# Performance work log

Measured on AMD Instinct MI355X. Metric: run time of the kernel, lower is better.

The kernel has to match this reference:

```python
import jax, jax.numpy as jnp
import numpy as np

B = 65536
N_SPARSE = 26
N_DENSE = 13
EMB = 5
VOCAB = 100000
N_EXPERTS = 4
D_IN = N_DENSE + N_SPARSE * EMB  # 143
H1, H2 = 128, 64


def setup_inputs() -> dict:
    key = jax.random.key(0)
    ks = jax.random.split(key, 16)
    s = 0.05
    return {
        "sparse_inputs": jax.random.randint(ks[0], (B, N_SPARSE), 0, VOCAB),
        "dense_inputs": jax.random.normal(ks[1], (B, N_DENSE), dtype=jnp.float32),
        "emb_tables": jax.random.normal(ks[2], (N_SPARSE, VOCAB, EMB), dtype=jnp.float32) * s,
        "expert_W1": jax.random.normal(ks[3], (N_EXPERTS, D_IN, H1), dtype=jnp.float32) * s,
        "expert_b1": jnp.zeros((N_EXPERTS, H1), dtype=jnp.float32),
        "expert_W2": jax.random.normal(ks[4], (N_EXPERTS, H1, H2), dtype=jnp.float32) * s,
        "expert_b2": jnp.zeros((N_EXPERTS, H2), dtype=jnp.float32),
        "gate_finish_W": jax.random.normal(ks[5], (D_IN, N_EXPERTS), dtype=jnp.float32) * s,
        "gate_finish_b": jnp.zeros((N_EXPERTS,), dtype=jnp.float32),
        "gate_like_W": jax.random.normal(ks[6], (D_IN, N_EXPERTS), dtype=jnp.float32) * s,
        "gate_like_b": jnp.zeros((N_EXPERTS,), dtype=jnp.float32),
        "finish_W": jax.random.normal(ks[7], (H2, 1), dtype=jnp.float32) * s,
        "finish_b": jnp.zeros((1,), dtype=jnp.float32),
        "like_W": jax.random.normal(ks[8], (H2, 1), dtype=jnp.float32) * s,
        "like_b": jnp.zeros((1,), dtype=jnp.float32),
    }


def reference(sparse_inputs, dense_inputs, emb_tables, expert_W1, expert_b1,
              expert_W2, expert_b2, gate_finish_W, gate_finish_b,
              gate_like_W, gate_like_b, finish_W, finish_b, like_W, like_b):
    # per-feature embedding lookup: [B, N_SPARSE, EMB]
    feat_idx = jnp.arange(N_SPARSE)[None, :]
    sp_emb = emb_tables[feat_idx, sparse_inputs]
    x = jnp.concatenate([dense_inputs, sp_emb.reshape(sparse_inputs.shape[0], -1)], axis=1)  # [B, D_IN]

    # batched expert MLPs (dropout is inactive at inference)
    h = jax.nn.relu(jnp.einsum('bd,edh->beh', x, expert_W1) + expert_b1)  # [B, E, 128]
    expert_out = jax.nn.relu(jnp.einsum('beh,eho->beo', h, expert_W2) + expert_b2)  # [B, E, 64]

    gate_f = jax.nn.softmax(x @ gate_finish_W + gate_finish_b, axis=-1)  # [B, E]
    gate_l = jax.nn.softmax(x @ gate_like_W + gate_like_b, axis=-1)

    task_finish = jnp.einsum('be,beo->bo', gate_f, expert_out)  # [B, 64]
    task_like = jnp.einsum('be,beo->bo', gate_l, expert_out)

    finish = jax.nn.sigmoid(task_finish @ finish_W + finish_b)  # [B, 1]
    like = jax.nn.sigmoid(task_like @ like_W + like_b)  # [B, 1]
    return finish, like
```

## Files before the change

### kernel.cpp

```cpp
#include <hip/hip_runtime.h>
#include <math.h>

#define NB     65536
#define NSP    26
#define NDN    13
#define EMBD   5
#define VOCAB  100000
#define NE     4
#define DIN    143
#define KPAD   160
#define H1     128
#define H2     64

typedef __attribute__((ext_vector_type(8))) short bf16x8;
typedef __attribute__((ext_vector_type(4))) float f32x4;

__device__ __forceinline__ unsigned short f2bf(float f) {
    unsigned int u = __float_as_uint(f);
    u = (u + 0x7fff + ((u >> 16) & 1)) >> 16;
    return (unsigned short)u;
}

__device__ __forceinline__ unsigned cvtpk(float lo, float hi) {
    unsigned r;
    asm("v_cvt_pk_bf16_f32 %0, %1, %2" : "=v"(r) : "v"(lo), "v"(hi));
    return r;
}

#define E1 (4*8*5*512)
#define E2 (4*4*4*512)
#define E3 (5*512)
#define NWE (E1+E2+E3)
#define GBLKS 1024
#define PBLKS ((NWE+255)/256)


__global__ __launch_bounds__(256)
void gather_pack(const int*   __restrict__ sparse,
                 const float* __restrict__ dense,
                 const float* __restrict__ emb,
                 const float* __restrict__ W1,  const float* __restrict__ W2,
                 const float* __restrict__ gfW, const float* __restrict__ glW,
                 unsigned short* __restrict__ w1p, unsigned short* __restrict__ w2p,
                 unsigned short* __restrict__ gwp, unsigned short* __restrict__ xg)
{
    const int blk = blockIdx.x;
    const int tid = threadIdx.x;
    if (blk < GBLKS) {
        __shared__ int idxs[64 * NSP];
        __shared__ __align__(16) unsigned short xs[64][168];
        const int row0 = blk * 64;

        for (int t = tid; t < 64 * NSP; t += 256)
            idxs[t] = sparse[row0 * NSP + t];
        for (int t = tid; t < 64 * NDN; t += 256) {
            int r = t / NDN, c = t - r * NDN;
            xs[r][c] = f2bf(dense[(row0 + r) * NDN + c]);
        }
        for (int t = tid; t < 64 * (KPAD - DIN); t += 256) {
            int r = t / (KPAD - DIN), c = DIN + (t - r * (KPAD - DIN));
            xs[r][c] = 0;
        }
        __syncthreads();
        for (int t = tid; t < 64 * NSP * EMBD; t += 256) {
            int f = t / (64 * EMBD);
            int rem = t - f * (64 * EMBD);
            int r = rem / EMBD, c = rem - r * EMBD;
            int idx = idxs[r * NSP + f];
            float v = emb[((size_t)f * VOCAB + idx) * EMBD + c];
            xs[r][NDN + f * EMBD + c] = f2bf(v);
        }
        __syncthreads();
        for (int v = tid; v < 4 * 5 * 64; v += 256) {
            int lo = v & 63, chunk = v >> 6;
            int s = chunk % 5, tl = chunk / 5;
            int b = lo & 15, g = lo >> 4;
            bf16x8 val = *(const bf16x8*)&xs[tl * 16 + b][32 * s + 8 * g];
            *(bf16x8*)(xg + ((size_t)((blk * 4 + tl) * 5 + s) * 64 + lo) * 8) = val;
        }
        return;
    }

    int i = (blk - GBLKS) * 256 + tid;
    if (i < E1) {
        int j = i & 7, l = (i >> 3) & 63;
        int rest = i >> 9;
        int s = rest % 5; rest /= 5;
        int nt = rest & 7, e = rest >> 3;
        int b = l & 15, g = l >> 4;
        int k = 32 * s + 8 * g + j;
        int n = nt * 16 + b;
        w1p[i] = (k < DIN) ? f2bf(W1[(e * DIN + k) * H1 + n]) : (unsigned short)0;
        return;
    }
    i -= E1;
    if (i < E2) {
        int j = i & 7, l = (i >> 3) & 63;
        int rest = i >> 9;
        int s = rest & 3; rest >>= 2;
        int ot = rest & 3, e = rest >> 2;
        int b = l & 15, g = l >> 4;
        int k = 32 * s + 8 * g + j;
        int o = ot * 16 + b;
        w2p[i] = f2bf(W2[(e * H1 + k) * H2 + o]);
        return;
    }
    i -= E2;
    if (i < E3) {
        int j = i & 7, l = (i >> 3) & 63;
        int s = i >> 9;
        int b = l & 15, g = l >> 4;
        int k = 32 * s + 8 * g + j;
        float v = 0.f;
        if (k < DIN) {
            if (b < 4)      v = gfW[k * NE + b];
            else if (b < 8) v = glW[k * NE + (b - 4)];
        }
        gwp[i] = f2bf(v);
    }
}

__global__ __launch_bounds__(256, 2)
void mmoe7(const unsigned short* __restrict__ xg,
           const unsigned short* __restrict__ w1p, const float* __restrict__ b1,
           const unsigned short* __restrict__ w2p, const float* __restrict__ b2,
           const unsigned short* __restrict__ gwp,
           const float* __restrict__ gfb, const float* __restrict__ glb,
           const float* __restrict__ fW,  const float* __restrict__ fb,
           const float* __restrict__ lW,  const float* __restrict__ lb,
           float* __restrict__ out)
{
    __shared__ __align__(16) char wlds[57344];
    __shared__ __align__(16) char hsb[16384];
    __shared__ float gts[128][8];

    const int tid  = threadIdx.x;
    const int wid  = tid >> 6;
    const int lane = tid & 63;
    const int b    = lane & 15;
    const int g    = lane >> 4;
    const int t0   = blockIdx.x * 8 + wid * 2;
    const int swz  = (b & 7) << 4;
    char* const hw = hsb + wid * 4096 + b * 128;

    bf16x8 xf[2][5];
    #pragma unroll
    for (int rt = 0; rt < 2; ++rt)
        #pragma unroll
        for (int s = 0; s < 5; ++s)
            xf[rt][s] = *(const bf16x8*)(xg + ((size_t)((t0 + rt) * 5 + s) * 64 + lane) * 8);

    bf16x8 pw1[10], pw2[4];
    #pragma unroll
    for (int i = 0; i < 10; ++i)
        pw1[i] = *(const bf16x8*)(w1p + (size_t)(tid + i * 256) * 8);
    #pragma unroll
    for (int i = 0; i < 4; ++i)
        pw2[i] = *(const bf16x8*)(w2p + (size_t)(tid + i * 256) * 8);

    f32x4 ga[2];
    ga[0] = (f32x4){0.f, 0.f, 0.f, 0.f};
    ga[1] = (f32x4){0.f, 0.f, 0.f, 0.f};
    #pragma unroll
    for (int s = 0; s < 5; ++s) {
        bf16x8 af = *(const bf16x8*)(gwp + (size_t)(s * 64 + lane) * 8);
        ga[0] = __builtin_amdgcn_mfma_f32_16x16x32_bf16(af, xf[0][s], ga[0], 0, 0, 0);
        ga[1] = __builtin_amdgcn_mfma_f32_16x16x32_bf16(af, xf[1][s], ga[1], 0, 0, 0);
    }
    if (g < 2) {
        const float4 bias = *(const float4*)(g ? glb : gfb);
        #pragma unroll
        for (int rt = 0; rt < 2; ++rt) {
            float l0 = ga[rt][0] + bias.x, l1 = ga[rt][1] + bias.y;
            float l2 = ga[rt][2] + bias.z, l3 = ga[rt][3] + bias.w;
            float m = fmaxf(fmaxf(l0, l1), fmaxf(l2, l3));
            float e0 = expf(l0 - m), e1 = expf(l1 - m), e2 = expf(l2 - m), e3 = expf(l3 - m);
            float inv = 1.f / (e0 + e1 + e2 + e3);
            float4 gv; gv.x = e0 * inv; gv.y = e1 * inv; gv.z = e2 * inv; gv.w = e3 * inv;
            *(float4*)&gts[wid * 32 + rt * 16 + b][g * 4] = gv;
        }
    }

    float vf[2] = {0.f, 0.f}, vl[2] = {0.f, 0.f};
    for (int e = 0; e < NE; ++e) {
        __syncthreads();
        #pragma unroll
        for (int i = 0; i < 10; ++i)
            *(bf16x8*)(wlds + (tid + i * 256) * 16) = pw1[i];
        #pragma unroll
        for (int i = 0; i < 4; ++i)
            *(bf16x8*)(wlds + 40960 + (tid + i * 256) * 16) = pw2[i];
        if (e < 3) {
            #pragma unroll
            for (int i = 0; i < 10; ++i)
                pw1[i] = *(const bf16x8*)(w1p + (size_t)(e + 1) * 20480 + (size_t)(tid + i * 256) * 8);
            #pragma unroll
            for (int i = 0; i < 4; ++i)
                pw2[i] = *(const bf16x8*)(w2p + (size_t)(e + 1) * 8192 + (size_t)(tid + i * 256) * 8);
        }
        __syncthreads();

        f32x4 c[2][4];
        #pragma unroll
        for (int rt = 0; rt < 2; ++rt)
            #pragma unroll
            for (int ot = 0; ot < 4; ++ot)
                c[rt][ot] = (f32x4){0.f, 0.f, 0.f, 0.f};

        #pragma unroll
        for (int h = 0; h < 2; ++h) {
            #pragma unroll
            for (int nl = 0; nl < 4; ++nl) {
                const int nt = h * 4 + nl;
                bf16x8 wv[5];
                #pragma unroll
                for (int s = 0; s < 5; ++s)
                    wv[s] = *(const bf16x8*)(wlds + ((nt * 5 + s) * 64 + lane) * 16);
                f32x4 acc[2];
                acc[0] = (f32x4){0.f, 0.f, 0.f, 0.f};
                acc[1] = (f32x4){0.f, 0.f, 0.f, 0.f};
                #pragma unroll
                for (int s = 0; s < 5; ++s) {
                    acc[0] = __builtin_amdgcn_mfma_f32_16x16x32_bf16(wv[s], xf[0][s], acc[0], 0, 0, 0);
                    acc[1] = __builtin_amdgcn_mfma_f32_16x16x32_bf16(wv[s], xf[1][s], acc[1], 0, 0, 0);
                }
                const float4 b1v = *(const float4*)(b1 + e * H1 + nt * 16 + 4 * g);
                #pragma unroll
                for (int rt = 0; rt < 2; ++rt) {
                    uint2 hv;
                    hv.x = cvtpk(fmaxf(acc[rt][0] + b1v.x, 0.f), fmaxf(acc[rt][1] + b1v.y, 0.f));
                    hv.y = cvtpk(fmaxf(acc[rt][2] + b1v.z, 0.f), fmaxf(acc[rt][3] + b1v.w, 0.f));
                    *(uint2*)(hw + rt * 2048 + ((nl * 32 + g * 8) ^ swz)) = hv;
                }
            }
            bf16x8 hf[2][2];
            #pragma unroll
            for (int sl = 0; sl < 2; ++sl)
                #pragma unroll
                for (int rt = 0; rt < 2; ++rt)
                    hf[sl][rt] = *(const bf16x8*)(hw + rt * 2048 + ((sl * 64 + g * 16) ^ swz));
            #pragma unroll
            for (int ot = 0; ot < 4; ++ot) {
                #pragma unroll
                for (int sl = 0; sl < 2; ++sl) {
                    bf16x8 wv2 = *(const bf16x8*)(wlds + 40960 + ((ot * 4 + h * 2 + sl) * 64 + lane) * 16);
                    c[0][ot] = __builtin_amdgcn_mfma_f32_16x16x32_bf16(wv2, hf[sl][0], c[0][ot], 0, 0, 0);
                    c[1][ot] = __builtin_amdgcn_mfma_f32_16x16x32_bf16(wv2, hf[sl][1], c[1][ot], 0, 0, 0);
                }
            }
        }

        float gfv[2], glv[2];
        #pragma unroll
        for (int rt = 0; rt < 2; ++rt) {
            gfv[rt] = gts[wid * 32 + rt * 16 + b][e];
            glv[rt] = gts[wid * 32 + rt * 16 + b][4 + e];
        }
        #pragma unroll
        for (int ot = 0; ot < 4; ++ot) {
            const float4 b2v = *(const float4*)(b2 + e * H2 + ot * 16 + 4 * g);
            const float4 fwv = *(const float4*)(fW + ot * 16 + 4 * g);
            const float4 lwv = *(const float4*)(lW + ot * 16 + 4 * g);
            #pragma unroll
            for (int rt = 0; rt < 2; ++rt) {
                float o0 = fmaxf(c[rt][ot][0] + b2v.x, 0.f), o1 = fmaxf(c[rt][ot][1] + b2v.y, 0.f);
                float o2 = fmaxf(c[rt][ot][2] + b2v.z, 0.f), o3 = fmaxf(c[rt][ot][3] + b2v.w, 0.f);
                vf[rt] += gfv[rt] * (o0 * fwv.x + o1 * fwv.y + o2 * fwv.z + o3 * fwv.w);
                vl[rt] += glv[rt] * (o0 * lwv.x + o1 * lwv.y + o2 * lwv.z + o3 * lwv.w);
            }
        }
    }

    #pragma unroll
    for (int rt = 0; rt < 2; ++rt) {
        float f = vf[rt], l = vl[rt];
        f += __shfl_xor(f, 16); f += __shfl_xor(f, 32);
        l += __shfl_xor(l, 16); l += __shfl_xor(l, 32);
        if (g == 0) {
            int r = (t0 + rt) * 16 + b;
            out[r]      = 1.f / (1.f + expf(-(f + fb[0])));
            out[NB + r] = 1.f / (1.f + expf(-(l + lb[0])));
        }
    }
}


__global__ __launch_bounds__(256)
void preproc(const float* __restrict__ W1, const float* __restrict__ W2,
             const float* __restrict__ gfW, const float* __restrict__ glW,
             unsigned short* __restrict__ w1t, unsigned short* __restrict__ w2t,
             unsigned short* __restrict__ gwc)
{
    int i = blockIdx.x * 256 + threadIdx.x;
    if (i < 4*128*160) {
        int k = i % KPAD;
        int n = (i / KPAD) & (H1 - 1);
        int e = i / (KPAD * H1);
        w1t[i] = (k < DIN) ? f2bf(W1[(e * DIN + k) * H1 + n]) : (unsigned short)0;
    } else if (i < 4*128*160 + 4*64*128) {
        int j = i - 4*128*160;
        int k = j & (H1 - 1);
        int o = (j >> 7) & (H2 - 1);
        int e = j >> 13;
        w2t[j] = f2bf(W2[(e * H1 + k) * H2 + o]);
    } else if (i < 4*128*160 + 4*64*128 + 16*160) {
        int j = i - (4*128*160 + 4*64*128);
        int k = j % KPAD;
        int r = j / KPAD;
        float v = 0.f;
        if (k < DIN) {
            if (r < 4)      v = gfW[k * NE + r];
            else if (r < 8) v = glW[k * NE + (r - 4)];
        }
        gwc[j] = f2bf(v);
    }
}

__global__ __launch_bounds__(256)
void mmoe_mfma(const int*   __restrict__ sparse,
               const float* __restrict__ dense,
               const float* __restrict__ emb,
               const unsigned short* __restrict__ w1t,
               const float* __restrict__ b1,
               const unsigned short* __restrict__ w2t,
               const float* __restrict__ b2,
               const unsigned short* __restrict__ gwc,
               const float* __restrict__ gfb, const float* __restrict__ glb,
               const float* __restrict__ fW,  const float* __restrict__ fb,
               const float* __restrict__ lW,  const float* __restrict__ lb,
               float* __restrict__ out)
{
    __shared__ __align__(16) unsigned short xs[64][KPAD];
    __shared__ __align__(16) unsigned short hs[64][136];
    __shared__ __align__(16) float gts[64][8];

    const int tid   = threadIdx.x;
    const int wid   = tid >> 6;
    const int lane  = tid & 63;
    const int b     = lane & 15;
    const int g     = lane >> 4;
    const int rbase = wid * 16;
    const int grow0 = blockIdx.x * 64 + rbase;

    for (int t = lane; t < 16 * NDN; t += 64) {
        int r = t & 15, d = t >> 4;
        xs[rbase + r][d] = f2bf(dense[(grow0 + r) * NDN + d]);
    }
    for (int t = lane; t < 16 * (KPAD - DIN); t += 64) {
        int r = t & 15, d = DIN + (t >> 4);
        xs[rbase + r][d] = 0;
    }
    for (int t = lane; t < 16 * NSP; t += 64) {
        int r = t & 15, f = t >> 4;
        int idx = sparse[(grow0 + r) * NSP + f];
        const float* ep = emb + (f * VOCAB + idx) * EMBD;
        int c0 = NDN + EMBD * f;
        #pragma unroll
        for (int c = 0; c < EMBD; ++c)
            xs[rbase + r][c0 + c] = f2bf(ep[c]);
    }

    bf16x8 xf[5];
    #pragma unroll
    for (int s = 0; s < 5; ++s)
        xf[s] = *(const bf16x8*)&xs[rbase + b][32 * s + 8 * g];

    f32x4 ga = {0.f, 0.f, 0.f, 0.f};
    #pragma unroll
    for (int s = 0; s < 5; ++s) {
        bf16x8 af = *(const bf16x8*)(gwc + b * KPAD + 32 * s + 8 * g);
        ga = __builtin_amdgcn_mfma_f32_16x16x32_bf16(af, xf[s], ga, 0, 0, 0);
    }
    if (g < 2) {
        const float4 bias = *(const float4*)(g ? glb : gfb);
        float l0 = ga[0] + bias.x, l1 = ga[1] + bias.y;
        float l2 = ga[2] + bias.z, l3 = ga[3] + bias.w;
        float m = fmaxf(fmaxf(l0, l1), fmaxf(l2, l3));
        float e0 = expf(l0 - m), e1 = expf(l1 - m), e2 = expf(l2 - m), e3 = expf(l3 - m);
        float inv = 1.f / (e0 + e1 + e2 + e3);
        float4 gv; gv.x = e0 * inv; gv.y = e1 * inv; gv.z = e2 * inv; gv.w = e3 * inv;
        *(float4*)&gts[rbase + b][g * 4] = gv;
    }

    float vf = 0.f, vl = 0.f;
    for (int e = 0; e < NE; ++e) {
        const unsigned short* w1e = w1t + e * (H1 * KPAD);
        #pragma unroll
        for (int nt = 0; nt < 8; ++nt) {
            f32x4 acc = {0.f, 0.f, 0.f, 0.f};
            #pragma unroll
            for (int s = 0; s < 5; ++s) {
                bf16x8 af = *(const bf16x8*)(w1e + (nt * 16 + b) * KPAD + 32 * s + 8 * g);
                acc = __builtin_amdgcn_mfma_f32_16x16x32_bf16(af, xf[s], acc, 0, 0, 0);
            }
            const float4 b1v = *(const float4*)(b1 + e * H1 + nt * 16 + 4 * g);
            unsigned lo = (unsigned)f2bf(fmaxf(acc[0] + b1v.x, 0.f)) |
                          ((unsigned)f2bf(fmaxf(acc[1] + b1v.y, 0.f)) << 16);
            unsigned hi = (unsigned)f2bf(fmaxf(acc[2] + b1v.z, 0.f)) |
                          ((unsigned)f2bf(fmaxf(acc[3] + b1v.w, 0.f)) << 16);
            uint2 hv; hv.x = lo; hv.y = hi;
            *(uint2*)&hs[rbase + b][nt * 16 + 4 * g] = hv;
        }

        bf16x8 hf[4];
        #pragma unroll
        for (int s = 0; s < 4; ++s)
            hf[s] = *(const bf16x8*)&hs[rbase + b][32 * s + 8 * g];

        float gf = gts[rbase + b][e];
        float gl = gts[rbase + b][4 + e];
        const unsigned short* w2e = w2t + e * (H2 * H1);
        #pragma unroll
        for (int ot = 0; ot < 4; ++ot) {
            f32x4 acc = {0.f, 0.f, 0.f, 0.f};
            #pragma unroll
            for (int s = 0; s < 4; ++s) {
                bf16x8 af = *(const bf16x8*)(w2e + (ot * 16 + b) * H1 + 32 * s + 8 * g);
                acc = __builtin_amdgcn_mfma_f32_16x16x32_bf16(af, hf[s], acc, 0, 0, 0);
            }
            const float4 b2v = *(const float4*)(b2 + e * H2 + ot * 16 + 4 * g);
            const float4 fwv = *(const float4*)(fW + ot * 16 + 4 * g);
            const float4 lwv = *(const float4*)(lW + ot * 16 + 4 * g);
            float o0 = fmaxf(acc[0] + b2v.x, 0.f);
            float o1 = fmaxf(acc[1] + b2v.y, 0.f);
            float o2 = fmaxf(acc[2] + b2v.z, 0.f);
            float o3 = fmaxf(acc[3] + b2v.w, 0.f);
            vf += gf * (o0 * fwv.x + o1 * fwv.y + o2 * fwv.z + o3 * fwv.w);
            vl += gl * (o0 * lwv.x + o1 * lwv.y + o2 * lwv.z + o3 * lwv.w);
        }
    }

    vf += __shfl_xor(vf, 16); vf += __shfl_xor(vf, 32);
    vl += __shfl_xor(vl, 16); vl += __shfl_xor(vl, 32);
    if (g == 0) {
        int r = grow0 + b;
        out[r]      = 1.f / (1.f + expf(-(vf + fb[0])));
        out[NB + r] = 1.f / (1.f + expf(-(vl + lb[0])));
    }
}


extern "C" void kernel_launch(void* const* d_in, const int* in_sizes, int n_in,
                              void* d_out, int out_size, void* d_ws, size_t ws_size,
                              hipStream_t stream) {
    const int*   sparse = (const int*)  d_in[0];
    const float* dense  = (const float*)d_in[1];
    const float* emb    = (const float*)d_in[2];
    const float* W1     = (const float*)d_in[3];
    const float* b1     = (const float*)d_in[4];
    const float* W2     = (const float*)d_in[5];
    const float* b2     = (const float*)d_in[6];
    const float* gfW    = (const float*)d_in[7];
    const float* gfb    = (const float*)d_in[8];
    const float* glW    = (const float*)d_in[9];
    const float* glb    = (const float*)d_in[10];
    const float* fW     = (const float*)d_in[11];
    const float* fb     = (const float*)d_in[12];
    const float* lW     = (const float*)d_in[13];
    const float* lb     = (const float*)d_in[14];

    const size_t XG_BYTES = (size_t)NB * KPAD * 2;
    const size_t NEED = XG_BYTES + (size_t)NWE * 2;

    if (ws_size >= NEED) {
        unsigned short* xg  = (unsigned short*)d_ws;
        unsigned short* w1p = (unsigned short*)((char*)d_ws + XG_BYTES);
        unsigned short* w2p = (unsigned short*)((char*)d_ws + XG_BYTES + (size_t)E1 * 2);
        unsigned short* gwp = (unsigned short*)((char*)d_ws + XG_BYTES + (size_t)(E1 + E2) * 2);

        gather_pack<<<GBLKS + PBLKS, 256, 0, stream>>>(
            sparse, dense, emb, W1, W2, gfW, glW, w1p, w2p, gwp, xg);
        mmoe7<<<NB / 128, 256, 0, stream>>>(xg, w1p, b1, w2p, b2, gwp,
                                            gfb, glb, fW, fb, lW, lb,
                                            (float*)d_out);
    } else {
        unsigned short* w1t = (unsigned short*)d_ws;
        unsigned short* w2t = (unsigned short*)((char*)d_ws + 163840);
        unsigned short* gwc = (unsigned short*)((char*)d_ws + 229376);

        int tot = 4*128*160 + 4*64*128 + 16*160;
        preproc<<<(tot + 255) / 256, 256, 0, stream>>>(W1, W2, gfW, glW, w1t, w2t, gwc);
        mmoe_mfma<<<NB / 64, 256, 0, stream>>>(sparse, dense, emb,
                                               w1t, b1, w2t, b2, gwc,
                                               gfb, glb, fW, fb, lW, lb,
                                               (float*)d_out);
    }
}
```

Before: 58.58 us.

## Stream W1 into LDS via global_load_lds and hold W2 in registers

Expert W1 tiles now go straight from global memory into LDS using global_load_lds, with no staging through registers. The next expert's W1 load is issued after the first GEMM finishes, so it overlaps the second GEMM. W2 fragments are read from global memory directly into registers each expert, and the full 128-wide hidden activation is written to LDS before one second-layer GEMM, instead of being processed in two halves. This cuts LDS footprint and register staging, but adds register pressure from 16 W2 fragments and a per-expert global W2 read in every wave.

```diff
diff --git a/kernel.cpp b/kernel.cpp
--- a/kernel.cpp
+++ b/kernel.cpp
@@ -25,6 +25,12 @@
     unsigned r;
     asm("v_cvt_pk_bf16_f32 %0, %1, %2" : "=v"(r) : "v"(lo), "v"(hi));
     return r;
+}
+
+__device__ __forceinline__ void gll16(const unsigned short* g, unsigned short* l) {
+    __builtin_amdgcn_global_load_lds(
+        (const __attribute__((address_space(1))) unsigned int*)g,
+        (__attribute__((address_space(3))) unsigned int*)l, 16, 0, 0);
 }
 
 #define E1 (4*8*5*512)
@@ -121,7 +127,7 @@
 }
 
 __global__ __launch_bounds__(256, 2)
-void mmoe7(const unsigned short* __restrict__ xg,
+void mmoe8(const unsigned short* __restrict__ xg,
            const unsigned short* __restrict__ w1p, const float* __restrict__ b1,
            const unsigned short* __restrict__ w2p, const float* __restrict__ b2,
            const unsigned short* __restrict__ gwp,
@@ -130,8 +136,8 @@
            const float* __restrict__ lW,  const float* __restrict__ lb,
            float* __restrict__ out)
 {
-    __shared__ __align__(16) char wlds[57344];
-    __shared__ __align__(16) char hsb[16384];
+    __shared__ __align__(16) unsigned short wlds[20480];
+    __shared__ __align__(16) char hsb[32768];
     __shared__ float gts[128][8];
 
     const int tid  = threadIdx.x;
@@ -141,7 +147,13 @@
     const int g    = lane >> 4;
     const int t0   = blockIdx.x * 8 + wid * 2;
     const int swz  = (b & 7) << 4;
-    char* const hw = hsb + wid * 4096 + b * 128;
+    char* const hw = hsb + wid * 8192 + b * 256;
+
+    #pragma unroll
+    for (int i = 0; i < 10; ++i) {
+        int c = wid * 10 + i;
+        gll16(w1p + ((size_t)c * 64 + lane) * 8, wlds + c * 512);
+    }
 
     bf16x8 xf[2][5];
     #pragma unroll
@@ -149,14 +161,6 @@
         #pragma unroll
         for (int s = 0; s < 5; ++s)
             xf[rt][s] = *(const bf16x8*)(xg + ((size_t)((t0 + rt) * 5 + s) * 64 + lane) * 8);
-
-    bf16x8 pw1[10], pw2[4];
-    #pragma unroll
-    for (int i = 0; i < 10; ++i)
-        pw1[i] = *(const bf16x8*)(w1p + (size_t)(tid + i * 256) * 8);
-    #pragma unroll
-    for (int i = 0; i < 4; ++i)
-        pw2[i] = *(const bf16x8*)(w2p + (size_t)(tid + i * 256) * 8);
 
     f32x4 ga[2];
     ga[0] = (f32x4){0.f, 0.f, 0.f, 0.f};
@@ -184,71 +188,52 @@
     float vf[2] = {0.f, 0.f}, vl[2] = {0.f, 0.f};
     for (int e = 0; e < NE; ++e) {
         __syncthreads();
-        #pragma unroll
-        for (int i = 0; i < 10; ++i)
-            *(bf16x8*)(wlds + (tid + i * 256) * 16) = pw1[i];
-        #pragma unroll
-        for (int i = 0; i < 4; ++i)
-            *(bf16x8*)(wlds + 40960 + (tid + i * 256) * 16) = pw2[i];
+
+        bf16x8 w2r[16];
+        #pragma unroll
+        for (int c2 = 0; c2 < 16; ++c2)
+            w2r[c2] = *(const bf16x8*)(w2p + (((size_t)e * 16 + c2) * 64 + lane) * 8);
+
+        #pragma unroll
+        for (int nt = 0; nt < 8; ++nt) {
+            bf16x8 wv[5];
+            #pragma unroll
+            for (int s = 0; s < 5; ++s)
+                wv[s] = *(const bf16x8*)(wlds + ((nt * 5 + s) * 64 + lane) * 8);
+            f32x4 acc[2];
+            acc[0] = (f32x4){0.f, 0.f, 0.f, 0.f};
+            acc[1] = (f32x4){0.f, 0.f, 0.f, 0.f};
+            #pragma unroll
+            for (int s = 0; s < 5; ++s) {
+                acc[0] = __builtin_amdgcn_mfma_f32_16x16x32_bf16(wv[s], xf[0][s], acc[0], 0, 0, 0);
+                acc[1] = __builtin_amdgcn_mfma_f32_16x16x32_bf16(wv[s], xf[1][s], acc[1], 0, 0, 0);
+            }
+            const float4 b1v = *(const float4*)(b1 + e * H1 + nt * 16 + 4 * g);
+            #pragma unroll
+            for (int rt = 0; rt < 2; ++rt) {
+                uint2 hv;
+                hv.x = cvtpk(fmaxf(acc[rt][0] + b1v.x, 0.f), fmaxf(acc[rt][1] + b1v.y, 0.f));
+                hv.y = cvtpk(fmaxf(acc[rt][2] + b1v.z, 0.f), fmaxf(acc[rt][3] + b1v.w, 0.f));
+                *(uint2*)(hw + rt * 4096 + ((nt * 32 + g * 8) ^ swz)) = hv;
+            }
+        }
+
+        __syncthreads();
+
         if (e < 3) {
             #pragma unroll
-            for (int i = 0; i < 10; ++i)
-                pw1[i] = *(const bf16x8*)(w1p + (size_t)(e + 1) * 20480 + (size_t)(tid + i * 256) * 8);
-            #pragma unroll
-            for (int i = 0; i < 4; ++i)
-                pw2[i] = *(const bf16x8*)(w2p + (size_t)(e + 1) * 8192 + (size_t)(tid + i * 256) * 8);
-        }
-        __syncthreads();
-
-        f32x4 c[2][4];
+            for (int i = 0; i < 10; ++i) {
+                int c2 = wid * 10 + i;
+                gll16(w1p + (((size_t)(e + 1) * 40 + c2) * 64 + lane) * 8, wlds + c2 * 512);
+            }
+        }
+
+        bf16x8 hf[2][4];
         #pragma unroll
         for (int rt = 0; rt < 2; ++rt)
             #pragma unroll
-            for (int ot = 0; ot < 4; ++ot)
-                c[rt][ot] = (f32x4){0.f, 0.f, 0.f, 0.f};
-
-        #pragma unroll
-        for (int h = 0; h < 2; ++h) {
-            #pragma unroll
-            for (int nl = 0; nl < 4; ++nl) {
-                const int nt = h * 4 + nl;
-                bf16x8 wv[5];
-                #pragma unroll
-                for (int s = 0; s < 5; ++s)
-                    wv[s] = *(const bf16x8*)(wlds + ((nt * 5 + s) * 64 + lane) * 16);
-                f32x4 acc[2];
-                acc[0] = (f32x4){0.f, 0.f, 0.f, 0.f};
-                acc[1] = (f32x4){0.f, 0.f, 0.f, 0.f};
-                #pragma unroll
-                for (int s = 0; s < 5; ++s) {
-                    acc[0] = __builtin_amdgcn_mfma_f32_16x16x32_bf16(wv[s], xf[0][s], acc[0], 0, 0, 0);
-                    acc[1] = __builtin_amdgcn_mfma_f32_16x16x32_bf16(wv[s], xf[1][s], acc[1], 0, 0, 0);
-                }
-                const float4 b1v = *(const float4*)(b1 + e * H1 + nt * 16 + 4 * g);
-                #pragma unroll
-                for (int rt = 0; rt < 2; ++rt) {
-                    uint2 hv;
-                    hv.x = cvtpk(fmaxf(acc[rt][0] + b1v.x, 0.f), fmaxf(acc[rt][1] + b1v.y, 0.f));
-                    hv.y = cvtpk(fmaxf(acc[rt][2] + b1v.z, 0.f), fmaxf(acc[rt][3] + b1v.w, 0.f));
-                    *(uint2*)(hw + rt * 2048 + ((nl * 32 + g * 8) ^ swz)) = hv;
-                }
-            }
-            bf16x8 hf[2][2];
-            #pragma unroll
-            for (int sl = 0; sl < 2; ++sl)
-                #pragma unroll
-                for (int rt = 0; rt < 2; ++rt)
-                    hf[sl][rt] = *(const bf16x8*)(hw + rt * 2048 + ((sl * 64 + g * 16) ^ swz));
-            #pragma unroll
-            for (int ot = 0; ot < 4; ++ot) {
-                #pragma unroll
-                for (int sl = 0; sl < 2; ++sl) {
-                    bf16x8 wv2 = *(const bf16x8*)(wlds + 40960 + ((ot * 4 + h * 2 + sl) * 64 + lane) * 16);
-                    c[0][ot] = __builtin_amdgcn_mfma_f32_16x16x32_bf16(wv2, hf[sl][0], c[0][ot], 0, 0, 0);
-                    c[1][ot] = __builtin_amdgcn_mfma_f32_16x16x32_bf16(wv2, hf[sl][1], c[1][ot], 0, 0, 0);
-                }
-            }
-        }
+            for (int s = 0; s < 4; ++s)
+                hf[rt][s] = *(const bf16x8*)(hw + rt * 4096 + ((s * 64 + g * 16) ^ swz));
 
         float gfv[2], glv[2];
         #pragma unroll
@@ -256,6 +241,20 @@
             gfv[rt] = gts[wid * 32 + rt * 16 + b][e];
             glv[rt] = gts[wid * 32 + rt * 16 + b][4 + e];
         }
+
+        f32x4 c[2][4];
+        #pragma unroll
+        for (int ot = 0; ot < 4; ++ot) {
+            c[0][ot] = (f32x4){0.f, 0.f, 0.f, 0.f};
+            c[1][ot] = (f32x4){0.f, 0.f, 0.f, 0.f};
+            #pragma unroll
+            for (int s = 0; s < 4; ++s) {
+                bf16x8 wv2 = w2r[ot * 4 + s];
+                c[0][ot] = __builtin_amdgcn_mfma_f32_16x16x32_bf16(wv2, hf[0][s], c[0][ot], 0, 0, 0);
+                c[1][ot] = __builtin_amdgcn_mfma_f32_16x16x32_bf16(wv2, hf[1][s], c[1][ot], 0, 0, 0);
+            }
+        }
+
         #pragma unroll
         for (int ot = 0; ot < 4; ++ot) {
             const float4 b2v = *(const float4*)(b2 + e * H2 + ot * 16 + 4 * g);
@@ -470,7 +469,7 @@
 
         gather_pack<<<GBLKS + PBLKS, 256, 0, stream>>>(
             sparse, dense, emb, W1, W2, gfW, glW, w1p, w2p, gwp, xg);
-        mmoe7<<<NB / 128, 256, 0, stream>>>(xg, w1p, b1, w2p, b2, gwp,
+        mmoe8<<<NB / 128, 256, 0, stream>>>(xg, w1p, b1, w2p, b2, gwp,
                                             gfb, glb, fW, fb, lW, lb,
                                             (float*)d_out);
     } else {
```

New measurement: 58.99 us, median of 2. Within noise of the previous version (+0.7%).

## Split experts across blocks with per-expert partial sums and epilogue kernel

Applied to the files above, without the earlier changes.

Each block of the MoE kernel now handles a single expert for its 128-row tile, launching four times as many blocks. Each block loads only that expert's weights into LDS once via global_load_lds, instead of cycling all four experts through registers and LDS with syncs in between. The gated partial head sums go to a workspace buffer, and a new small kernel adds them and applies the sigmoid. This raises parallelism and shrinks LDS use for better occupancy. In exchange, every block reloads its input tile, gate MFMAs are recomputed four times per row, and there is an extra kernel launch plus an extra global round trip.

```diff
diff --git a/kernel.cpp b/kernel.cpp
--- a/kernel.cpp
+++ b/kernel.cpp
@@ -25,6 +25,12 @@
     unsigned r;
     asm("v_cvt_pk_bf16_f32 %0, %1, %2" : "=v"(r) : "v"(lo), "v"(hi));
     return r;
+}
+
+__device__ __forceinline__ void gll16(const unsigned short* g, unsigned short* l) {
+    __builtin_amdgcn_global_load_lds(
+        (const __attribute__((address_space(1))) unsigned int*)g,
+        (__attribute__((address_space(3))) unsigned int*)l, 16, 0, 0);
 }
 
 #define E1 (4*8*5*512)
@@ -121,42 +127,44 @@
 }
 
 __global__ __launch_bounds__(256, 2)
-void mmoe7(const unsigned short* __restrict__ xg,
+void mmoe9(const unsigned short* __restrict__ xg,
            const unsigned short* __restrict__ w1p, const float* __restrict__ b1,
            const unsigned short* __restrict__ w2p, const float* __restrict__ b2,
            const unsigned short* __restrict__ gwp,
            const float* __restrict__ gfb, const float* __restrict__ glb,
-           const float* __restrict__ fW,  const float* __restrict__ fb,
-           const float* __restrict__ lW,  const float* __restrict__ lb,
-           float* __restrict__ out)
+           const float* __restrict__ fW,  const float* __restrict__ lW,
+           float* __restrict__ acc)
 {
-    __shared__ __align__(16) char wlds[57344];
+    __shared__ __align__(16) unsigned short wlds[28672];
     __shared__ __align__(16) char hsb[16384];
-    __shared__ float gts[128][8];
 
     const int tid  = threadIdx.x;
     const int wid  = tid >> 6;
     const int lane = tid & 63;
     const int b    = lane & 15;
     const int g    = lane >> 4;
-    const int t0   = blockIdx.x * 8 + wid * 2;
+    const int rg   = blockIdx.x >> 2;
+    const int e    = blockIdx.x & 3;
+    const int t0   = rg * 8 + wid * 2;
     const int swz  = (b & 7) << 4;
     char* const hw = hsb + wid * 4096 + b * 128;
 
+    #pragma unroll
+    for (int i = 0; i < 14; ++i) {
+        int c = wid * 14 + i;
+        if (c < 40)
+            gll16(w1p + (((size_t)e * 40 + c) * 64 + lane) * 8, wlds + c * 512);
+        else
+            gll16(w2p + (((size_t)e * 16 + (c - 40)) * 64 + lane) * 8,
+                  wlds + 20480 + (c - 40) * 512);
+    }
+
     bf16x8 xf[2][5];
     #pragma unroll
     for (int rt = 0; rt < 2; ++rt)
         #pragma unroll
         for (int s = 0; s < 5; ++s)
             xf[rt][s] = *(const bf16x8*)(xg + ((size_t)((t0 + rt) * 5 + s) * 64 + lane) * 8);
-
-    bf16x8 pw1[10], pw2[4];
-    #pragma unroll
-    for (int i = 0; i < 10; ++i)
-        pw1[i] = *(const bf16x8*)(w1p + (size_t)(tid + i * 256) * 8);
-    #pragma unroll
-    for (int i = 0; i < 4; ++i)
-        pw2[i] = *(const bf16x8*)(w2p + (size_t)(tid + i * 256) * 8);
 
     f32x4 ga[2];
     ga[0] = (f32x4){0.f, 0.f, 0.f, 0.f};
@@ -167,107 +175,87 @@
         ga[0] = __builtin_amdgcn_mfma_f32_16x16x32_bf16(af, xf[0][s], ga[0], 0, 0, 0);
         ga[1] = __builtin_amdgcn_mfma_f32_16x16x32_bf16(af, xf[1][s], ga[1], 0, 0, 0);
     }
-    if (g < 2) {
-        const float4 bias = *(const float4*)(g ? glb : gfb);
+    const float4 gfb4 = *(const float4*)gfb;
+    const float4 glb4 = *(const float4*)glb;
+    float gfv[2], glv[2];
+    #pragma unroll
+    for (int rt = 0; rt < 2; ++rt) {
+        const float4 bias = (g == 1) ? glb4 : gfb4;
+        float l0 = ga[rt][0] + bias.x, l1 = ga[rt][1] + bias.y;
+        float l2 = ga[rt][2] + bias.z, l3 = ga[rt][3] + bias.w;
+        float m = fmaxf(fmaxf(l0, l1), fmaxf(l2, l3));
+        float e0 = expf(l0 - m), e1 = expf(l1 - m), e2 = expf(l2 - m), e3 = expf(l3 - m);
+        float inv = 1.f / (e0 + e1 + e2 + e3);
+        float sel = (e == 0) ? e0 : (e == 1) ? e1 : (e == 2) ? e2 : e3;
+        sel *= inv;
+        gfv[rt] = __shfl(sel, b);
+        glv[rt] = __shfl(sel, b + 16);
+    }
+
+    __syncthreads();
+
+    float vf[2] = {0.f, 0.f}, vl[2] = {0.f, 0.f};
+    f32x4 c[2][4];
+    #pragma unroll
+    for (int rt = 0; rt < 2; ++rt)
+        #pragma unroll
+        for (int ot = 0; ot < 4; ++ot)
+            c[rt][ot] = (f32x4){0.f, 0.f, 0.f, 0.f};
+
+    #pragma unroll
+    for (int h = 0; h < 2; ++h) {
+        #pragma unroll
+        for (int nl = 0; nl < 4; ++nl) {
+            const int nt = h * 4 + nl;
+            bf16x8 wv[5];
+            #pragma unroll
+            for (int s = 0; s < 5; ++s)
+                wv[s] = *(const bf16x8*)(wlds + ((nt * 5 + s) * 64 + lane) * 8);
+            f32x4 a2[2];
+            a2[0] = (f32x4){0.f, 0.f, 0.f, 0.f};
+            a2[1] = (f32x4){0.f, 0.f, 0.f, 0.f};
+            #pragma unroll
+            for (int s = 0; s < 5; ++s) {
+                a2[0] = __builtin_amdgcn_mfma_f32_16x16x32_bf16(wv[s], xf[0][s], a2[0], 0, 0, 0);
+                a2[1] = __builtin_amdgcn_mfma_f32_16x16x32_bf16(wv[s], xf[1][s], a2[1], 0, 0, 0);
+            }
+            const float4 b1v = *(const float4*)(b1 + e * H1 + nt * 16 + 4 * g);
+            #pragma unroll
+            for (int rt = 0; rt < 2; ++rt) {
+                uint2 hv;
+                hv.x = cvtpk(fmaxf(a2[rt][0] + b1v.x, 0.f), fmaxf(a2[rt][1] + b1v.y, 0.f));
+                hv.y = cvtpk(fmaxf(a2[rt][2] + b1v.z, 0.f), fmaxf(a2[rt][3] + b1v.w, 0.f));
+                *(uint2*)(hw + rt * 2048 + ((nl * 32 + g * 8) ^ swz)) = hv;
+            }
+        }
+        bf16x8 hf[2][2];
+        #pragma unroll
+        for (int sl = 0; sl < 2; ++sl)
+            #pragma unroll
+            for (int rt = 0; rt < 2; ++rt)
+                hf[sl][rt] = *(const bf16x8*)(hw + rt * 2048 + ((sl * 64 + g * 16) ^ swz));
+        #pragma unroll
+        for (int ot = 0; ot < 4; ++ot) {
+            #pragma unroll
+            for (int sl = 0; sl < 2; ++sl) {
+                bf16x8 wv2 = *(const bf16x8*)(wlds + 20480 + ((ot * 4 + h * 2 + sl) * 64 + lane) * 8);
+                c[0][ot] = __builtin_amdgcn_mfma_f32_16x16x32_bf16(wv2, hf[sl][0], c[0][ot], 0, 0, 0);
+                c[1][ot] = __builtin_amdgcn_mfma_f32_16x16x32_bf16(wv2, hf[sl][1], c[1][ot], 0, 0, 0);
+            }
+        }
+    }
+
+    #pragma unroll
+    for (int ot = 0; ot < 4; ++ot) {
+        const float4 b2v = *(const float4*)(b2 + e * H2 + ot * 16 + 4 * g);
+        const float4 fwv = *(const float4*)(fW + ot * 16 + 4 * g);
+        const float4 lwv = *(const float4*)(lW + ot * 16 + 4 * g);
         #pragma unroll
         for (int rt = 0; rt < 2; ++rt) {
-            float l0 = ga[rt][0] + bias.x, l1 = ga[rt][1] + bias.y;
-            float l2 = ga[rt][2] + bias.z, l3 = ga[rt][3] + bias.w;
-            float m = fmaxf(fmaxf(l0, l1), fmaxf(l2, l3));
-            float e0 = expf(l0 - m), e1 = expf(l1 - m), e2 = expf(l2 - m), e3 = expf(l3 - m);
-            float inv = 1.f / (e0 + e1 + e2 + e3);
-            float4 gv; gv.x = e0 * inv; gv.y = e1 * inv; gv.z = e2 * inv; gv.w = e3 * inv;
-            *(float4*)&gts[wid * 32 + rt * 16 + b][g * 4] = gv;
-        }
-    }
-
-    float vf[2] = {0.f, 0.f}, vl[2] = {0.f, 0.f};
-    for (int e = 0; e < NE; ++e) {
-        __syncthreads();
-        #pragma unroll
-        for (int i = 0; i < 10; ++i)
-            *(bf16x8*)(wlds + (tid + i * 256) * 16) = pw1[i];
-        #pragma unroll
-        for (int i = 0; i < 4; ++i)
-            *(bf16x8*)(wlds + 40960 + (tid + i * 256) * 16) = pw2[i];
-        if (e < 3) {
-            #pragma unroll
-            for (int i = 0; i < 10; ++i)
-                pw1[i] = *(const bf16x8*)(w1p + (size_t)(e + 1) * 20480 + (size_t)(tid + i * 256) * 8);
-            #pragma unroll
-            for (int i = 0; i < 4; ++i)
-                pw2[i] = *(const bf16x8*)(w2p + (size_t)(e + 1) * 8192 + (size_t)(tid + i * 256) * 8);
-        }
-        __syncthreads();
-
-        f32x4 c[2][4];
-        #pragma unroll
-        for (int rt = 0; rt < 2; ++rt)
-            #pragma unroll
-            for (int ot = 0; ot < 4; ++ot)
-                c[rt][ot] = (f32x4){0.f, 0.f, 0.f, 0.f};
-
-        #pragma unroll
-        for (int h = 0; h < 2; ++h) {
-            #pragma unroll
-            for (int nl = 0; nl < 4; ++nl) {
-                const int nt = h * 4 + nl;
-                bf16x8 wv[5];
-                #pragma unroll
-                for (int s = 0; s < 5; ++s)
-                    wv[s] = *(const bf16x8*)(wlds + ((nt * 5 + s) * 64 + lane) * 16);
-                f32x4 acc[2];
-                acc[0] = (f32x4){0.f, 0.f, 0.f, 0.f};
-                acc[1] = (f32x4){0.f, 0.f, 0.f, 0.f};
-                #pragma unroll
-                for (int s = 0; s < 5; ++s) {
-                    acc[0] = __builtin_amdgcn_mfma_f32_16x16x32_bf16(wv[s], xf[0][s], acc[0], 0, 0, 0);
-                    acc[1] = __builtin_amdgcn_mfma_f32_16x16x32_bf16(wv[s], xf[1][s], acc[1], 0, 0, 0);
-                }
-                const float4 b1v = *(const float4*)(b1 + e * H1 + nt * 16 + 4 * g);
-                #pragma unroll
-                for (int rt = 0; rt < 2; ++rt) {
-                    uint2 hv;
-                    hv.x = cvtpk(fmaxf(acc[rt][0] + b1v.x, 0.f), fmaxf(acc[rt][1] + b1v.y, 0.f));
-                    hv.y = cvtpk(fmaxf(acc[rt][2] + b1v.z, 0.f), fmaxf(acc[rt][3] + b1v.w, 0.f));
-                    *(uint2*)(hw + rt * 2048 + ((nl * 32 + g * 8) ^ swz)) = hv;
-                }
-            }
-            bf16x8 hf[2][2];
-            #pragma unroll
-            for (int sl = 0; sl < 2; ++sl)
-                #pragma unroll
-                for (int rt = 0; rt < 2; ++rt)
-                    hf[sl][rt] = *(const bf16x8*)(hw + rt * 2048 + ((sl * 64 + g * 16) ^ swz));
-            #pragma unroll
-            for (int ot = 0; ot < 4; ++ot) {
-                #pragma unroll
-                for (int sl = 0; sl < 2; ++sl) {
-                    bf16x8 wv2 = *(const bf16x8*)(wlds + 40960 + ((ot * 4 + h * 2 + sl) * 64 + lane) * 16);
-                    c[0][ot] = __builtin_amdgcn_mfma_f32_16x16x32_bf16(wv2, hf[sl][0], c[0][ot], 0, 0, 0);
-                    c[1][ot] = __builtin_amdgcn_mfma_f32_16x16x32_bf16(wv2, hf[sl][1], c[1][ot], 0, 0, 0);
-                }
-            }
-        }
-
-        float gfv[2], glv[2];
-        #pragma unroll
-        for (int rt = 0; rt < 2; ++rt) {
-            gfv[rt] = gts[wid * 32 + rt * 16 + b][e];
-            glv[rt] = gts[wid * 32 + rt * 16 + b][4 + e];
-        }
-        #pragma unroll
-        for (int ot = 0; ot < 4; ++ot) {
-            const float4 b2v = *(const float4*)(b2 + e * H2 + ot * 16 + 4 * g);
-            const float4 fwv = *(const float4*)(fW + ot * 16 + 4 * g);
-            const float4 lwv = *(const float4*)(lW + ot * 16 + 4 * g);
-            #pragma unroll
-            for (int rt = 0; rt < 2; ++rt) {
-                float o0 = fmaxf(c[rt][ot][0] + b2v.x, 0.f), o1 = fmaxf(c[rt][ot][1] + b2v.y, 0.f);
-                float o2 = fmaxf(c[rt][ot][2] + b2v.z, 0.f), o3 = fmaxf(c[rt][ot][3] + b2v.w, 0.f);
-                vf[rt] += gfv[rt] * (o0 * fwv.x + o1 * fwv.y + o2 * fwv.z + o3 * fwv.w);
-                vl[rt] += glv[rt] * (o0 * lwv.x + o1 * lwv.y + o2 * lwv.z + o3 * lwv.w);
-            }
+            float o0 = fmaxf(c[rt][ot][0] + b2v.x, 0.f), o1 = fmaxf(c[rt][ot][1] + b2v.y, 0.f);
+            float o2 = fmaxf(c[rt][ot][2] + b2v.z, 0.f), o3 = fmaxf(c[rt][ot][3] + b2v.w, 0.f);
+            vf[rt] += gfv[rt] * (o0 * fwv.x + o1 * fwv.y + o2 * fwv.z + o3 * fwv.w);
+            vl[rt] += glv[rt] * (o0 * lwv.x + o1 * lwv.y + o2 * lwv.z + o3 * lwv.w);
         }
     }
 
@@ -278,10 +266,22 @@
         l += __shfl_xor(l, 16); l += __shfl_xor(l, 32);
         if (g == 0) {
             int r = (t0 + rt) * 16 + b;
-            out[r]      = 1.f / (1.f + expf(-(f + fb[0])));
-            out[NB + r] = 1.f / (1.f + expf(-(l + lb[0])));
-        }
-    }
+            acc[(size_t)e * NB + r]            = f;
+            acc[(size_t)(4 + e) * NB + r]      = l;
+        }
+    }
+}
+
+__global__ __launch_bounds__(256)
+void heads_ep(const float* __restrict__ acc,
+              const float* __restrict__ fb, const float* __restrict__ lb,
+              float* __restrict__ out)
+{
+    int r = blockIdx.x * 256 + threadIdx.x;
+    float sf = acc[r] + acc[NB + r] + acc[2 * NB + r] + acc[3 * NB + r];
+    float sl = acc[4 * NB + r] + acc[5 * NB + r] + acc[6 * NB + r] + acc[7 * NB + r];
+    out[r]      = 1.f / (1.f + expf(-(sf + fb[0])));
+    out[NB + r] = 1.f / (1.f + expf(-(sl + lb[0])));
 }
 
 
@@ -459,20 +459,23 @@
     const float* lW     = (const float*)d_in[13];
     const float* lb     = (const float*)d_in[14];
 
-    const size_t XG_BYTES = (size_t)NB * KPAD * 2;
-    const size_t NEED = XG_BYTES + (size_t)NWE * 2;
+    const size_t XG_BYTES  = (size_t)NB * KPAD * 2;
+    const size_t W_BYTES   = (size_t)NWE * 2;
+    const size_t ACC_BYTES = (size_t)2 * 4 * NB * 4;
+    const size_t NEED = XG_BYTES + W_BYTES + ACC_BYTES;
 
     if (ws_size >= NEED) {
         unsigned short* xg  = (unsigned short*)d_ws;
         unsigned short* w1p = (unsigned short*)((char*)d_ws + XG_BYTES);
         unsigned short* w2p = (unsigned short*)((char*)d_ws + XG_BYTES + (size_t)E1 * 2);
         unsigned short* gwp = (unsigned short*)((char*)d_ws + XG_BYTES + (size_t)(E1 + E2) * 2);
+        float*          acc = (float*)((char*)d_ws + XG_BYTES + W_BYTES);
 
         gather_pack<<<GBLKS + PBLKS, 256, 0, stream>>>(
             sparse, dense, emb, W1, W2, gfW, glW, w1p, w2p, gwp, xg);
-        mmoe7<<<NB / 128, 256, 0, stream>>>(xg, w1p, b1, w2p, b2, gwp,
-                                            gfb, glb, fW, fb, lW, lb,
-                                            (float*)d_out);
+        mmoe9<<<(NB / 128) * 4, 256, 0, stream>>>(xg, w1p, b1, w2p, b2, gwp,
+                                                  gfb, glb, fW, lW, acc);
+        heads_ep<<<NB / 256, 256, 0, stream>>>(acc, fb, lb, (float*)d_out);
     } else {
         unsigned short* w1t = (unsigned short*)d_ws;
         unsigned short* w2t = (unsigned short*)((char*)d_ws + 163840);
```

New measurement: 68.57 us. 1.17x slower.
